# Kernel optimization log

Measured on AMD Instinct MI355X. Metric: run time of the kernel, lower is better.

## Reference

```python
import jax, jax.numpy as jnp
import numpy as np

B, S, D, H = 2, 2048, 1024, 16
DEPTH = D // H
NEG = -1e9

def setup_inputs() -> dict:
    key = jax.random.key(0)
    k = jax.random.split(key, 4)
    return {
        "token_inputs": jax.random.normal(k[0], (B, S, D), dtype=jnp.float32),
        "mask": jnp.zeros((B, 1, 1, S), dtype=jnp.float32),
        "W_qkv": jax.random.normal(k[1], (D, 3 * D), dtype=jnp.float32) * 0.02,
        "b_qkv": jnp.zeros((3 * D,), dtype=jnp.float32),
        "W_out": jax.random.normal(k[2], (D, D), dtype=jnp.float32) * 0.02,
        "b_out": jnp.zeros((D,), dtype=jnp.float32),
    }

def reference(token_inputs, mask, W_qkv, b_qkv, W_out, b_out):
    # fused QKV projection
    qkv = token_inputs @ W_qkv + b_qkv                       # [B,S,3D]
    q, k, v = jnp.split(qkv, 3, axis=-1)                     # [B,S,D] each
    # split heads -> [B,H,S,depth]
    split = lambda x: x.reshape(B, S, H, DEPTH).transpose(0, 2, 1, 3)
    q, k, v = split(q), split(k), split(v)
    # causal additive mask: 0 on/below diagonal, -1e9 above
    causal = (1.0 - jnp.tril(jnp.ones((S, S), dtype=jnp.float32))) * NEG
    full_mask = mask + causal                                # [B,1,S,S]
    # scaled dot-product attention
    scores = jnp.einsum('bhqd,bhkd->bhqk', q, k) / jnp.sqrt(jnp.float32(DEPTH))
    scores = scores + full_mask
    attn = jax.nn.softmax(scores, axis=-1)                   # [B,H,S,S]
    ctx = jnp.einsum('bhqk,bhkd->bhqd', attn, v)             # [B,H,S,depth]
    # merge heads and final projection
    ctx = ctx.transpose(0, 2, 1, 3).reshape(B, S, D)
    return ctx @ W_out + b_out
```

## Files before the change

### kernel.cpp

```cpp
#include <hip/hip_runtime.h>
#include <hip/hip_bf16.h>

#define B_ 2
#define S_ 2048
#define D_ 1024
#define H_ 16
#define DEPTH_ 64

typedef __attribute__((ext_vector_type(4))) float f32x4;
typedef __attribute__((ext_vector_type(16))) float f32x16;
typedef __attribute__((ext_vector_type(8))) short bf16x8;
typedef __attribute__((ext_vector_type(2))) int i32x2;
typedef const __attribute__((address_space(1))) unsigned int gu32;
typedef __attribute__((address_space(3))) unsigned int lu32;

__device__ __forceinline__ void gload_lds16(const void* g, void* l) {
  __builtin_amdgcn_global_load_lds((gu32*)g, (lu32*)l, 16, 0, 0);
}

__device__ __forceinline__ short f2bf(float f) {
  union { float f; unsigned u; } v; v.f = f;
  return (short)((v.u + 0x7FFFu + ((v.u >> 16) & 1u)) >> 16);
}
__device__ __forceinline__ unsigned pk2(float lo, float hi) {
  unsigned r;
  asm("v_cvt_pk_bf16_f32 %0, %1, %2" : "=v"(r) : "v"(lo), "v"(hi));
  return r;
}
__device__ __forceinline__ i32x2 plswap(unsigned a, unsigned b) {
  return __builtin_amdgcn_permlane32_swap((int)a, (int)b, false, false);
}
#define BARRIER_RAW() do {                      \
  __builtin_amdgcn_sched_barrier(0);            \
  asm volatile("" ::: "memory");                \
  __builtin_amdgcn_s_barrier();                 \
  asm volatile("" ::: "memory");                \
  __builtin_amdgcn_sched_barrier(0);            \
} while (0)

__global__ __launch_bounds__(256) void cast_kernel(const float* __restrict__ in,
                                                   short* __restrict__ out, int n4) {
  int i = blockIdx.x * 256 + threadIdx.x;
  if (i < n4) {
    const float4 v = reinterpret_cast<const float4*>(in)[i];
    short2 a, b;
    *reinterpret_cast<unsigned*>(&a) = pk2(v.x, v.y);
    *reinterpret_cast<unsigned*>(&b) = pk2(v.z, v.w);
    reinterpret_cast<short4*>(out)[i] = make_short4(a.x, a.y, b.x, b.y);
  }
}

__global__ __launch_bounds__(256) void transpose_cast_kernel(const float* __restrict__ W,
                                                             short* __restrict__ WT,
                                                             int K, int N) {
  __shared__ short tile[32][33];
  int n0 = blockIdx.x * 32, k0 = blockIdx.y * 32;
  int tx = threadIdx.x, ty = threadIdx.y;
#pragma unroll
  for (int j = 0; j < 4; ++j)
    tile[ty + 8 * j][tx] = f2bf(W[(size_t)(k0 + ty + 8 * j) * N + n0 + tx]);
  __syncthreads();
#pragma unroll
  for (int j = 0; j < 4; ++j)
    WT[(size_t)(n0 + ty + 8 * j) * K + k0 + tx] = tile[tx][ty + 8 * j];
}

template <int EPI, int BM>
__global__ __launch_bounds__(512) void gemm_bt_kernel(
    const short* __restrict__ A, const short* __restrict__ BT,
    const float* __restrict__ bias,
    short* __restrict__ Qh, short* __restrict__ Kh, short* __restrict__ VTt,
    float* __restrict__ Out, int M, int N, int K) {
  constexpr int MI = BM / 64;
  constexpr int ASZ = BM * 32;
  constexpr int BSZ = 128 * 32;
  __shared__ short smem[2 * ASZ + 2 * BSZ];
  const int bm = blockIdx.y * BM, bn = blockIdx.x * 128;
  const int tid = threadIdx.x;
  const int w = tid >> 6, lane = tid & 63;
  const int wr = w >> 1, wc = w & 1;
  const int lr = lane & 15, lg = lane >> 4;
  const int s_r = lane >> 2, s_c = (lane & 3) * 8;
  f32x4 acc[MI][4] = {};
  const int nk = K >> 5;

  auto stage = [&](int buf, int kt) {
    short* Asb = smem + (buf ? ASZ : 0);
    short* Bsb = smem + 2 * ASZ + (buf ? BSZ : 0);
    if (BM == 128 || w < 4)
      gload_lds16(&A[(size_t)(bm + 16 * w + s_r) * K + kt * 32 + s_c], &Asb[16 * w * 32]);
    gload_lds16(&BT[(size_t)(bn + 16 * w + s_r) * K + kt * 32 + s_c], &Bsb[16 * w * 32]);
  };

  stage(0, 0);
  asm volatile("s_waitcnt vmcnt(0)" ::: "memory");
  BARRIER_RAW();
  int cur = 0;
  for (int kt = 0; kt < nk; ++kt) {
    if (kt + 1 < nk) {
      stage(cur ^ 1, kt + 1);
      if (BM == 128 || w < 4) asm volatile("s_waitcnt vmcnt(2)" ::: "memory");
      else                    asm volatile("s_waitcnt vmcnt(1)" ::: "memory");
    } else {
      asm volatile("s_waitcnt vmcnt(0)" ::: "memory");
    }
    BARRIER_RAW();
    const short* Asb = smem + (cur ? ASZ : 0);
    const short* Bsb = smem + 2 * ASZ + (cur ? BSZ : 0);
    bf16x8 af[MI], bfr[4];
#pragma unroll
    for (int mi = 0; mi < MI; ++mi)
      af[mi] = *reinterpret_cast<const bf16x8*>(&Asb[((BM / 4) * wr + 16 * mi + lr) * 32 + 8 * lg]);
#pragma unroll
    for (int ni = 0; ni < 4; ++ni)
      bfr[ni] = *reinterpret_cast<const bf16x8*>(&Bsb[(64 * wc + 16 * ni + lr) * 32 + 8 * lg]);
#pragma unroll
    for (int mi = 0; mi < MI; ++mi)
#pragma unroll
      for (int ni = 0; ni < 4; ++ni)
        acc[mi][ni] = __builtin_amdgcn_mfma_f32_16x16x32_bf16(af[mi], bfr[ni], acc[mi][ni], 0, 0, 0);
    BARRIER_RAW();
    cur ^= 1;
  }

  if constexpr (EPI == 0) {
    if (bn >= 2 * D_) {
      __syncthreads();
      short* vt = smem;
#pragma unroll
      for (int mi = 0; mi < MI; ++mi)
#pragma unroll
        for (int ni = 0; ni < 4; ++ni)
#pragma unroll
          for (int r = 0; r < 4; r += 2) {
            int row_local = (BM / 4) * wr + 16 * mi + 4 * lg + r;
            int col_local = 64 * wc + 16 * ni + lr;
            float bv = bias[bn + col_local];
            unsigned u = pk2(acc[mi][ni][r] + bv, acc[mi][ni][r + 1] + bv);
            int rsw = row_local ^ ((col_local & 7) << 3);
            *reinterpret_cast<unsigned*>(&vt[col_local * 128 + rsw]) = u;
          }
      __syncthreads();
      const int b = bm >> 11, sbase = bm & (S_ - 1);
#pragma unroll
      for (int p = 0; p < 4; ++p) {
        int slot = 512 * p + tid;
        int vrow = slot >> 4, seg = slot & 15;
        int dd_col = bn - 2 * D_ + vrow;
        int hh = dd_col >> 6, dd = dd_col & 63;
        int csw = (seg * 8) ^ ((vrow & 7) << 3);
        short* dst = &VTt[((size_t)(b * H_ + hh) * DEPTH_ + dd) * S_ + sbase + seg * 8];
        *reinterpret_cast<bf16x8*>(dst) = *reinterpret_cast<const bf16x8*>(&vt[vrow * 128 + csw]);
      }
    } else {
      constexpr float SCQ = 0.125f * 1.44269504f;
#pragma unroll
      for (int mi = 0; mi < MI; ++mi)
#pragma unroll
        for (int ni = 0; ni < 4; ++ni)
#pragma unroll
          for (int r = 0; r < 4; ++r) {
            int row = bm + (BM / 4) * wr + 16 * mi + 4 * lg + r;
            int col = bn + 64 * wc + 16 * ni + lr;
            float v = acc[mi][ni][r] + bias[col];
            int b = row >> 11, s = row & (S_ - 1);
            int which = col >> 10, cm = col & (D_ - 1);
            int hh = cm >> 6, dd = cm & 63;
            size_t bh = (size_t)(b * H_ + hh);
            if (which == 0) Qh[(bh * S_ + s) * DEPTH_ + dd] = f2bf(v * SCQ);
            else            Kh[(bh * S_ + s) * DEPTH_ + dd] = f2bf(v);
          }
    }
  } else {
#pragma unroll
    for (int mi = 0; mi < MI; ++mi)
#pragma unroll
      for (int ni = 0; ni < 4; ++ni)
#pragma unroll
        for (int r = 0; r < 4; ++r) {
          int row = bm + (BM / 4) * wr + 16 * mi + 4 * lg + r;
          int col = bn + 64 * wc + 16 * ni + lr;
          Out[(size_t)row * N + col] = acc[mi][ni][r] + bias[col];
        }
  }
}

__global__ __launch_bounds__(256, 4) void attn_kernel(
    const short* __restrict__ Qh, const short* __restrict__ Kh,
    const short* __restrict__ VTt, const float* __restrict__ mask,
    short* __restrict__ ctx) {
  constexpr float LOG2E = 1.44269504f;
  __shared__ short smem[16384];
  const int bid = blockIdx.x;
  const int j = bid >> 5, g = j & 7, rr = j >> 3;
  const int qt = (rr == 0) ? 31 - g : (rr == 1) ? 16 + g : (rr == 2) ? 15 - g : g;
  const int bh = bid & 31;
  const int b = bh >> 4, h = bh & 15;
  const short* Qp = Qh + (size_t)bh * S_ * DEPTH_;
  const short* Kp = Kh + (size_t)bh * S_ * DEPTH_;
  const short* Vp = VTt + (size_t)bh * DEPTH_ * S_;
  const int tid = threadIdx.x;
  const int w = tid >> 6, lane = tid & 63;
  const int sw = w & 1, ch = w >> 1;
  const int lq = lane & 31, hi = lane >> 5;
  const int q0w = qt * 64 + sw * 32;
  const int scs = 8 * ((lane & 7) ^ ((lane >> 3) & 7));
  const int srw = lane >> 3;
  short* Ksc = smem + ch * 8192;
  short* Vsc = Ksc + 4096;

  bf16x8 qf[4];
#pragma unroll
  for (int ksd = 0; ksd < 4; ++ksd)
    qf[ksd] = *reinterpret_cast<const bf16x8*>(&Qp[(size_t)(q0w + lq) * DEPTH_ + 16 * ksd + 8 * hi]);

  bf16x8 ones = {};
  if (hi == 0) ones[0] = (short)0x3F80;

  f32x16 acc0 = {}, acc1 = {};
  float l_run = 0.f;

  const int nt = qt + 1;
  const int nh = (nt + 1) >> 1;
  for (int i = 0; i < nh; ++i) {
    const int kt = ch ? (nh + i) : i;
    const bool valid = kt < nt;
    const int k0 = kt * 64;
    __syncthreads();
    if (valid) {
#pragma unroll
      for (int jj = 0; jj < 4; ++jj) {
        const int brow = sw * 32 + jj * 8;
        gload_lds16(&Kp[(size_t)(k0 + brow + srw) * DEPTH_ + scs], &Ksc[brow * 64]);
        gload_lds16(&Vp[(size_t)(brow + srw) * S_ + k0 + scs], &Vsc[brow * 64]);
      }
    }
    __syncthreads();
    if (!valid) continue;

    f32x16 sc[2] = {{}, {}};
#pragma unroll
    for (int h2 = 0; h2 < 2; ++h2) {
#pragma unroll
      for (int ksd = 0; ksd < 4; ++ksd) {
        const int row = h2 * 32 + lq;
        const int col = (16 * ksd + 8 * hi) ^ ((row & 7) * 8);
        bf16x8 kf = *reinterpret_cast<const bf16x8*>(&Ksc[row * 64 + col]);
        sc[h2] = __builtin_amdgcn_mfma_f32_32x32x16_bf16(kf, qf[ksd], sc[h2], 0, 0, 0);
      }
      float mv = mask[(size_t)b * S_ + k0 + h2 * 32 + lq];
      bf16x8 maf = {};
      if (hi == 0) maf[0] = f2bf(LOG2E * mv);
      sc[h2] = __builtin_amdgcn_mfma_f32_32x32x16_bf16(maf, ones, sc[h2], 0, 0, 0);
    }
    if (kt == nt - 1) {
      const int qg = q0w + lq;
#pragma unroll
      for (int h2 = 0; h2 < 2; ++h2)
#pragma unroll
        for (int r = 0; r < 16; ++r) {
          int kvg = k0 + (r & 3) + 8 * (r >> 2) + 4 * hi + 32 * h2;
          if (kvg > qg) sc[h2][r] = -1e30f;
        }
    }
#pragma unroll
    for (int h2 = 0; h2 < 2; ++h2)
#pragma unroll
      for (int r = 0; r < 16; ++r) sc[h2][r] = exp2f(sc[h2][r]);
    float s8[8];
#pragma unroll
    for (int r = 0; r < 8; ++r) s8[r] = (sc[0][r] + sc[0][r + 8]) + (sc[1][r] + sc[1][r + 8]);
#pragma unroll
    for (int r = 0; r < 4; ++r) s8[r] = s8[r] + s8[r + 4];
    float su = (s8[0] + s8[1]) + (s8[2] + s8[3]);
    {
      union { float f; int i; } sb; sb.f = su;
      i32x2 rs = plswap((unsigned)sb.i, (unsigned)sb.i);
      union { int i; float f; } p0, p1; p0.i = rs[0]; p1.i = rs[1];
      l_run += p0.f + p1.f;
    }

#pragma unroll
    for (int h2 = 0; h2 < 2; ++h2) {
#pragma unroll
      for (int ks = 0; ks < 2; ++ks) {
        const int rb = 8 * ks;
        unsigned a = pk2(sc[h2][rb + 0], sc[h2][rb + 1]);
        unsigned bq = pk2(sc[h2][rb + 2], sc[h2][rb + 3]);
        unsigned c = pk2(sc[h2][rb + 4], sc[h2][rb + 5]);
        unsigned d = pk2(sc[h2][rb + 6], sc[h2][rb + 7]);
        i32x2 r02 = plswap(a, c);
        i32x2 r13 = plswap(bq, d);
        union { unsigned u[4]; bf16x8 v; } pf;
        pf.u[0] = (unsigned)r02[0];
        pf.u[1] = (unsigned)r13[0];
        pf.u[2] = (unsigned)r02[1];
        pf.u[3] = (unsigned)r13[1];
#pragma unroll
        for (int dh = 0; dh < 2; ++dh) {
          const int row = dh * 32 + lq;
          const int col = (32 * h2 + 16 * ks + 8 * hi) ^ ((row & 7) * 8);
          bf16x8 vf = *reinterpret_cast<const bf16x8*>(&Vsc[row * 64 + col]);
          if (dh == 0) acc0 = __builtin_amdgcn_mfma_f32_32x32x16_bf16(vf, pf.v, acc0, 0, 0, 0);
          else         acc1 = __builtin_amdgcn_mfma_f32_32x32x16_bf16(vf, pf.v, acc1, 0, 0, 0);
        }
      }
    }
  }

  __syncthreads();
  float* F  = (float*)smem;
  float* ML = (float*)(smem + 8192);
  short* ob = smem + 8704;
  if (ch == 1) {
    float* dst = F + ((size_t)sw * 64 + lane) * 32;
#pragma unroll
    for (int r = 0; r < 16; ++r) { dst[r] = acc0[r]; dst[16 + r] = acc1[r]; }
    ML[sw * 64 + lane] = l_run;
  }
  __syncthreads();
  if (ch == 0) {
    const float* src = F + ((size_t)sw * 64 + lane) * 32;
    const float rl = 1.f / (l_run + ML[sw * 64 + lane]);
#pragma unroll
    for (int r = 0; r < 16; ++r) {
      acc0[r] = (acc0[r] + src[r]) * rl;
      acc1[r] = (acc1[r] + src[16 + r]) * rl;
    }
#pragma unroll
    for (int dh = 0; dh < 2; ++dh) {
      const f32x16& Aa = dh ? acc1 : acc0;
#pragma unroll
      for (int gg = 0; gg < 4; ++gg)
#pragma unroll
        for (int p = 0; p < 2; ++p) {
          int r0 = 4 * gg + 2 * p;
          int d0 = 2 * p + 8 * gg + 4 * hi + 32 * dh;
          unsigned u = pk2(Aa[r0], Aa[r0 + 1]);
          *reinterpret_cast<unsigned*>(&ob[(sw * 32 + lq) * 72 + d0]) = u;
        }
    }
  }
  __syncthreads();
  {
    const int row = tid >> 2, seg = tid & 3;
    short* dst = ctx + ((size_t)b * S_ + qt * 64 + row) * D_ + h * 64 + seg * 16;
    const short* srcp = &ob[row * 72 + seg * 16];
    *reinterpret_cast<bf16x8*>(dst) = *reinterpret_cast<const bf16x8*>(srcp);
    *reinterpret_cast<bf16x8*>(dst + 8) = *reinterpret_cast<const bf16x8*>(srcp + 8);
  }
}

extern "C" void kernel_launch(void* const* d_in, const int* in_sizes, int n_in,
                              void* d_out, int out_size, void* d_ws, size_t ws_size,
                              hipStream_t stream) {
  const float* X    = (const float*)d_in[0];
  const float* mask = (const float*)d_in[1];
  const float* Wqkv = (const float*)d_in[2];
  const float* bqkv = (const float*)d_in[3];
  const float* Wout = (const float*)d_in[4];
  const float* bout = (const float*)d_in[5];
  float* Out = (float*)d_out;

  short* ws    = (short*)d_ws;
  short* Xb    = ws;
  short* WqkvT = Xb + (size_t)4096 * 1024;
  short* WoutT = WqkvT + (size_t)3072 * 1024;
  short* Qh    = WoutT + (size_t)1024 * 1024;
  short* Kh    = Qh + (size_t)B_ * H_ * S_ * DEPTH_;
  short* VTt   = Kh + (size_t)B_ * H_ * S_ * DEPTH_;
  short* ctx   = VTt + (size_t)B_ * H_ * S_ * DEPTH_;

  cast_kernel<<<4096, 256, 0, stream>>>(X, Xb, (4096 * 1024) / 4);
  transpose_cast_kernel<<<dim3(96, 32), dim3(32, 8), 0, stream>>>(Wqkv, WqkvT, 1024, 3072);
  transpose_cast_kernel<<<dim3(32, 32), dim3(32, 8), 0, stream>>>(Wout, WoutT, 1024, 1024);
  gemm_bt_kernel<0, 128><<<dim3(24, 32), 512, 0, stream>>>(Xb, WqkvT, bqkv, Qh, Kh, VTt, nullptr,
                                                           4096, 3072, 1024);
  attn_kernel<<<1024, 256, 0, stream>>>(Qh, Kh, VTt, mask, ctx);
  gemm_bt_kernel<1, 64><<<dim3(8, 64), 512, 0, stream>>>(ctx, WoutT, bout, nullptr, nullptr, nullptr,
                                                         Out, 4096, 1024, 1024);
}
```

Baseline: 110.1 us.

## Split attention into 32-row query blocks with 4-way KV split, fuse prep kernels

The attention kernel now gives each block 32 query rows instead of 64, doubling the grid, and splits the KV range four ways across warps. Each warp loads its own 32-key K chunk and a shared swizzled V region. Partial accumulators are reduced through LDS at the end. The three cast/transpose prep kernels are merged into a single launch. The aim is better load balance and occupancy for the causal triangle and fewer launches, at the cost of a larger cross-warp reduction and lower reuse of K/V per loaded tile.

```diff
diff --git a/kernel.cpp b/kernel.cpp
--- a/kernel.cpp
+++ b/kernel.cpp
@@ -38,31 +38,37 @@
   __builtin_amdgcn_sched_barrier(0);            \
 } while (0)
 
-__global__ __launch_bounds__(256) void cast_kernel(const float* __restrict__ in,
-                                                   short* __restrict__ out, int n4) {
-  int i = blockIdx.x * 256 + threadIdx.x;
-  if (i < n4) {
-    const float4 v = reinterpret_cast<const float4*>(in)[i];
+__global__ __launch_bounds__(256) void prep_kernel(
+    const float* __restrict__ X, short* __restrict__ Xb,
+    const float* __restrict__ Wqkv, short* __restrict__ WqkvT,
+    const float* __restrict__ Wout, short* __restrict__ WoutT) {
+  __shared__ short tile[32][33];
+  const int bid = blockIdx.x, tid = threadIdx.x;
+  if (bid < 4096) {
+    int i = bid * 256 + tid;
+    const float4 v = reinterpret_cast<const float4*>(X)[i];
     short2 a, b;
     *reinterpret_cast<unsigned*>(&a) = pk2(v.x, v.y);
     *reinterpret_cast<unsigned*>(&b) = pk2(v.z, v.w);
-    reinterpret_cast<short4*>(out)[i] = make_short4(a.x, a.y, b.x, b.y);
-  }
-}
-
-__global__ __launch_bounds__(256) void transpose_cast_kernel(const float* __restrict__ W,
-                                                             short* __restrict__ WT,
-                                                             int K, int N) {
-  __shared__ short tile[32][33];
-  int n0 = blockIdx.x * 32, k0 = blockIdx.y * 32;
-  int tx = threadIdx.x, ty = threadIdx.y;
-#pragma unroll
-  for (int j = 0; j < 4; ++j)
-    tile[ty + 8 * j][tx] = f2bf(W[(size_t)(k0 + ty + 8 * j) * N + n0 + tx]);
-  __syncthreads();
-#pragma unroll
-  for (int j = 0; j < 4; ++j)
-    WT[(size_t)(n0 + ty + 8 * j) * K + k0 + tx] = tile[tx][ty + 8 * j];
+    reinterpret_cast<short4*>(Xb)[i] = make_short4(a.x, a.y, b.x, b.y);
+  } else {
+    const float* W;
+    short* WT;
+    int N, tb;
+    if (bid < 7168) { W = Wqkv; WT = WqkvT; N = 3072; tb = bid - 4096; }
+    else            { W = Wout; WT = WoutT; N = 1024; tb = bid - 7168; }
+    const int K = 1024;
+    const int nblk = N >> 5;
+    const int n0 = (tb % nblk) * 32, k0 = (tb / nblk) * 32;
+    const int tx = tid & 31, ty = tid >> 5;
+#pragma unroll
+    for (int j = 0; j < 4; ++j)
+      tile[ty + 8 * j][tx] = f2bf(W[(size_t)(k0 + ty + 8 * j) * N + n0 + tx]);
+    __syncthreads();
+#pragma unroll
+    for (int j = 0; j < 4; ++j)
+      WT[(size_t)(n0 + ty + 8 * j) * K + k0 + tx] = tile[tx][ty + 8 * j];
+  }
 }
 
 template <int EPI, int BM>
@@ -192,8 +198,7 @@
   constexpr float LOG2E = 1.44269504f;
   __shared__ short smem[16384];
   const int bid = blockIdx.x;
-  const int j = bid >> 5, g = j & 7, rr = j >> 3;
-  const int qt = (rr == 0) ? 31 - g : (rr == 1) ? 16 + g : (rr == 2) ? 15 - g : g;
+  const int ss = 63 - (bid >> 5);
   const int bh = bid & 31;
   const int b = bh >> 4, h = bh & 15;
   const short* Qp = Qh + (size_t)bh * S_ * DEPTH_;
@@ -201,13 +206,18 @@
   const short* Vp = VTt + (size_t)bh * DEPTH_ * S_;
   const int tid = threadIdx.x;
   const int w = tid >> 6, lane = tid & 63;
-  const int sw = w & 1, ch = w >> 1;
   const int lq = lane & 31, hi = lane >> 5;
-  const int q0w = qt * 64 + sw * 32;
-  const int scs = 8 * ((lane & 7) ^ ((lane >> 3) & 7));
+  const int q0w = ss * 32;
+  const int nt = ss + 1;
+  const int base = nt >> 2, rem = nt & 3;
+  const int mycnt = base + (w < rem ? 1 : 0);
+  const int mystart = w * base + (w < rem ? w : rem);
+  const int mc = base + (rem ? 1 : 0);
+  short* KR = smem;
+  short* VR = smem + 8192;
   const int srw = lane >> 3;
-  short* Ksc = smem + ch * 8192;
-  short* Vsc = Ksc + 4096;
+  const int scs = 8 * ((lane & 7) ^ srw);
+  const int vps = lane & 15;
 
   bf16x8 qf[4];
 #pragma unroll
@@ -220,56 +230,58 @@
   f32x16 acc0 = {}, acc1 = {};
   float l_run = 0.f;
 
-  const int nt = qt + 1;
-  const int nh = (nt + 1) >> 1;
-  for (int i = 0; i < nh; ++i) {
-    const int kt = ch ? (nh + i) : i;
-    const bool valid = kt < nt;
-    const int k0 = kt * 64;
+  for (int i = 0; i < mc; ++i) {
     __syncthreads();
-    if (valid) {
-#pragma unroll
-      for (int jj = 0; jj < 4; ++jj) {
-        const int brow = sw * 32 + jj * 8;
-        gload_lds16(&Kp[(size_t)(k0 + brow + srw) * DEPTH_ + scs], &Ksc[brow * 64]);
-        gload_lds16(&Vp[(size_t)(brow + srw) * S_ + k0 + scs], &Vsc[brow * 64]);
+    if (i < mycnt) {
+      const int kc = mystart + i;
+#pragma unroll
+      for (int jj = 0; jj < 4; ++jj)
+        gload_lds16(&Kp[(size_t)(kc * 32 + jj * 8 + srw) * DEPTH_ + scs],
+                    &KR[(w * 32 + jj * 8) * 64]);
+    }
+#pragma unroll
+    for (int jj = 0; jj < 4; ++jj) {
+      const int r = w * 16 + jj * 4 + (lane >> 4);
+      const int ls = vps ^ (r & 7);
+      const int c = ls >> 2, g8 = ls & 3;
+      const int ccnt = base + (c < rem ? 1 : 0);
+      const int cstart = c * base + (c < rem ? c : rem);
+      if (i < ccnt) {
+        const int kc = cstart + i;
+        gload_lds16(&Vp[(size_t)r * S_ + kc * 32 + g8 * 8], &VR[(w * 16 + jj * 4) * 128]);
       }
     }
     __syncthreads();
-    if (!valid) continue;
-
-    f32x16 sc[2] = {{}, {}};
-#pragma unroll
-    for (int h2 = 0; h2 < 2; ++h2) {
-#pragma unroll
-      for (int ksd = 0; ksd < 4; ++ksd) {
-        const int row = h2 * 32 + lq;
-        const int col = (16 * ksd + 8 * hi) ^ ((row & 7) * 8);
-        bf16x8 kf = *reinterpret_cast<const bf16x8*>(&Ksc[row * 64 + col]);
-        sc[h2] = __builtin_amdgcn_mfma_f32_32x32x16_bf16(kf, qf[ksd], sc[h2], 0, 0, 0);
-      }
-      float mv = mask[(size_t)b * S_ + k0 + h2 * 32 + lq];
+    if (i >= mycnt) continue;
+
+    const int kt = mystart + i;
+    const int k0 = kt * 32;
+    f32x16 sc = {};
+#pragma unroll
+    for (int ksd = 0; ksd < 4; ++ksd) {
+      bf16x8 kf = *reinterpret_cast<const bf16x8*>(
+          &KR[(w * 32 + lq) * 64 + ((16 * ksd + 8 * hi) ^ ((lq & 7) * 8))]);
+      sc = __builtin_amdgcn_mfma_f32_32x32x16_bf16(kf, qf[ksd], sc, 0, 0, 0);
+    }
+    {
+      float mv = mask[(size_t)b * S_ + k0 + lq];
       bf16x8 maf = {};
       if (hi == 0) maf[0] = f2bf(LOG2E * mv);
-      sc[h2] = __builtin_amdgcn_mfma_f32_32x32x16_bf16(maf, ones, sc[h2], 0, 0, 0);
+      sc = __builtin_amdgcn_mfma_f32_32x32x16_bf16(maf, ones, sc, 0, 0, 0);
     }
     if (kt == nt - 1) {
       const int qg = q0w + lq;
 #pragma unroll
-      for (int h2 = 0; h2 < 2; ++h2)
-#pragma unroll
-        for (int r = 0; r < 16; ++r) {
-          int kvg = k0 + (r & 3) + 8 * (r >> 2) + 4 * hi + 32 * h2;
-          if (kvg > qg) sc[h2][r] = -1e30f;
-        }
-    }
-#pragma unroll
-    for (int h2 = 0; h2 < 2; ++h2)
-#pragma unroll
-      for (int r = 0; r < 16; ++r) sc[h2][r] = exp2f(sc[h2][r]);
+      for (int r = 0; r < 16; ++r) {
+        int kvg = k0 + (r & 3) + 8 * (r >> 2) + 4 * hi;
+        if (kvg > qg) sc[r] = -1e30f;
+      }
+    }
+#pragma unroll
+    for (int r = 0; r < 16; ++r) sc[r] = exp2f(sc[r]);
     float s8[8];
 #pragma unroll
-    for (int r = 0; r < 8; ++r) s8[r] = (sc[0][r] + sc[0][r + 8]) + (sc[1][r] + sc[1][r + 8]);
+    for (int r = 0; r < 8; ++r) s8[r] = sc[r] + sc[r + 8];
 #pragma unroll
     for (int r = 0; r < 4; ++r) s8[r] = s8[r] + s8[r + 4];
     float su = (s8[0] + s8[1]) + (s8[2] + s8[3]);
@@ -279,54 +291,52 @@
       union { int i; float f; } p0, p1; p0.i = rs[0]; p1.i = rs[1];
       l_run += p0.f + p1.f;
     }
-
-#pragma unroll
-    for (int h2 = 0; h2 < 2; ++h2) {
-#pragma unroll
-      for (int ks = 0; ks < 2; ++ks) {
-        const int rb = 8 * ks;
-        unsigned a = pk2(sc[h2][rb + 0], sc[h2][rb + 1]);
-        unsigned bq = pk2(sc[h2][rb + 2], sc[h2][rb + 3]);
-        unsigned c = pk2(sc[h2][rb + 4], sc[h2][rb + 5]);
-        unsigned d = pk2(sc[h2][rb + 6], sc[h2][rb + 7]);
-        i32x2 r02 = plswap(a, c);
-        i32x2 r13 = plswap(bq, d);
-        union { unsigned u[4]; bf16x8 v; } pf;
-        pf.u[0] = (unsigned)r02[0];
-        pf.u[1] = (unsigned)r13[0];
-        pf.u[2] = (unsigned)r02[1];
-        pf.u[3] = (unsigned)r13[1];
-#pragma unroll
-        for (int dh = 0; dh < 2; ++dh) {
-          const int row = dh * 32 + lq;
-          const int col = (32 * h2 + 16 * ks + 8 * hi) ^ ((row & 7) * 8);
-          bf16x8 vf = *reinterpret_cast<const bf16x8*>(&Vsc[row * 64 + col]);
-          if (dh == 0) acc0 = __builtin_amdgcn_mfma_f32_32x32x16_bf16(vf, pf.v, acc0, 0, 0, 0);
-          else         acc1 = __builtin_amdgcn_mfma_f32_32x32x16_bf16(vf, pf.v, acc1, 0, 0, 0);
-        }
+#pragma unroll
+    for (int ks = 0; ks < 2; ++ks) {
+      const int rb = 8 * ks;
+      unsigned a = pk2(sc[rb + 0], sc[rb + 1]);
+      unsigned bq = pk2(sc[rb + 2], sc[rb + 3]);
+      unsigned c = pk2(sc[rb + 4], sc[rb + 5]);
+      unsigned d = pk2(sc[rb + 6], sc[rb + 7]);
+      i32x2 r02 = plswap(a, c);
+      i32x2 r13 = plswap(bq, d);
+      union { unsigned u[4]; bf16x8 v; } pf;
+      pf.u[0] = (unsigned)r02[0];
+      pf.u[1] = (unsigned)r13[0];
+      pf.u[2] = (unsigned)r02[1];
+      pf.u[3] = (unsigned)r13[1];
+#pragma unroll
+      for (int dh = 0; dh < 2; ++dh) {
+        const int row = dh * 32 + lq;
+        const int ps = (4 * w + 2 * ks + hi) ^ (row & 7);
+        bf16x8 vf = *reinterpret_cast<const bf16x8*>(&VR[row * 128 + ps * 8]);
+        if (dh == 0) acc0 = __builtin_amdgcn_mfma_f32_32x32x16_bf16(vf, pf.v, acc0, 0, 0, 0);
+        else         acc1 = __builtin_amdgcn_mfma_f32_32x32x16_bf16(vf, pf.v, acc1, 0, 0, 0);
       }
     }
   }
 
   __syncthreads();
   float* F  = (float*)smem;
-  float* ML = (float*)(smem + 8192);
-  short* ob = smem + 8704;
-  if (ch == 1) {
-    float* dst = F + ((size_t)sw * 64 + lane) * 32;
+  float* Lp = (float*)(smem + 12288);
+  short* ob = smem + 12672;
+  if (w != 0) {
+    float* dst = F + ((size_t)(w - 1) * 64 + lane) * 32;
 #pragma unroll
     for (int r = 0; r < 16; ++r) { dst[r] = acc0[r]; dst[16 + r] = acc1[r]; }
-    ML[sw * 64 + lane] = l_run;
+    Lp[(w - 1) * 64 + lane] = l_run;
   }
   __syncthreads();
-  if (ch == 0) {
-    const float* src = F + ((size_t)sw * 64 + lane) * 32;
-    const float rl = 1.f / (l_run + ML[sw * 64 + lane]);
-#pragma unroll
-    for (int r = 0; r < 16; ++r) {
-      acc0[r] = (acc0[r] + src[r]) * rl;
-      acc1[r] = (acc1[r] + src[16 + r]) * rl;
-    }
+  if (w == 0) {
+    float lt = l_run;
+#pragma unroll
+    for (int s = 0; s < 3; ++s) {
+      const float* src = F + ((size_t)s * 64 + lane) * 32;
+      lt += Lp[s * 64 + lane];
+#pragma unroll
+      for (int r = 0; r < 16; ++r) { acc0[r] += src[r]; acc1[r] += src[16 + r]; }
+    }
+    const float rl = 1.f / lt;
 #pragma unroll
     for (int dh = 0; dh < 2; ++dh) {
       const f32x16& Aa = dh ? acc1 : acc0;
@@ -336,18 +346,16 @@
         for (int p = 0; p < 2; ++p) {
           int r0 = 4 * gg + 2 * p;
           int d0 = 2 * p + 8 * gg + 4 * hi + 32 * dh;
-          unsigned u = pk2(Aa[r0], Aa[r0 + 1]);
-          *reinterpret_cast<unsigned*>(&ob[(sw * 32 + lq) * 72 + d0]) = u;
+          unsigned u = pk2(Aa[r0] * rl, Aa[r0 + 1] * rl);
+          *reinterpret_cast<unsigned*>(&ob[lq * 72 + d0]) = u;
         }
     }
   }
   __syncthreads();
   {
-    const int row = tid >> 2, seg = tid & 3;
-    short* dst = ctx + ((size_t)b * S_ + qt * 64 + row) * D_ + h * 64 + seg * 16;
-    const short* srcp = &ob[row * 72 + seg * 16];
-    *reinterpret_cast<bf16x8*>(dst) = *reinterpret_cast<const bf16x8*>(srcp);
-    *reinterpret_cast<bf16x8*>(dst + 8) = *reinterpret_cast<const bf16x8*>(srcp + 8);
+    const int row = tid >> 3, seg = tid & 7;
+    short* dst = ctx + ((size_t)b * S_ + q0w + row) * D_ + h * 64 + seg * 8;
+    *reinterpret_cast<bf16x8*>(dst) = *reinterpret_cast<const bf16x8*>(&ob[row * 72 + seg * 8]);
   }
 }
 
@@ -371,12 +379,10 @@
   short* VTt   = Kh + (size_t)B_ * H_ * S_ * DEPTH_;
   short* ctx   = VTt + (size_t)B_ * H_ * S_ * DEPTH_;
 
-  cast_kernel<<<4096, 256, 0, stream>>>(X, Xb, (4096 * 1024) / 4);
-  transpose_cast_kernel<<<dim3(96, 32), dim3(32, 8), 0, stream>>>(Wqkv, WqkvT, 1024, 3072);
-  transpose_cast_kernel<<<dim3(32, 32), dim3(32, 8), 0, stream>>>(Wout, WoutT, 1024, 1024);
+  prep_kernel<<<8192, 256, 0, stream>>>(X, Xb, Wqkv, WqkvT, Wout, WoutT);
   gemm_bt_kernel<0, 128><<<dim3(24, 32), 512, 0, stream>>>(Xb, WqkvT, bqkv, Qh, Kh, VTt, nullptr,
                                                            4096, 3072, 1024);
-  attn_kernel<<<1024, 256, 0, stream>>>(Qh, Kh, VTt, mask, ctx);
+  attn_kernel<<<2048, 256, 0, stream>>>(Qh, Kh, VTt, mask, ctx);
   gemm_bt_kernel<1, 64><<<dim3(8, 64), 512, 0, stream>>>(ctx, WoutT, bout, nullptr, nullptr, nullptr,
                                                          Out, 4096, 1024, 1024);
 }
```

Result: slower. 114.7 us (+4.2%).
